# Optimization experiments

Measured on AMD Instinct MI355X. Metric: run time of the kernel, lower is better.

Reference implementation:

```python
import jax, jax.numpy as jnp
import numpy as np


def _mw_weight(m):
    if m == 1:
        return 1j * np.pi / 2
    if m == -1:
        return -1j * np.pi / 2
    if m % 2 == 0:
        return 2.0 / (1 - m * m)
    return 0.0


def quad_weights_mw(L):
    # Exact MW quadrature weights (McEwen & Wiaux 2011), folded to L theta samples.
    ms = np.arange(-(L - 1), L)
    w = np.array([_mw_weight(m) for m in ms], dtype=np.complex128)
    w *= np.exp(-1j * ms * np.pi / (2 * L - 1))
    wr = np.real(np.fft.fft(np.fft.ifftshift(w))) / (2 * L - 1)
    q = wr[:L].copy()
    q[: L - 1] += wr[2 * L - 2 : L - 1 : -1]  # fold extended-grid weights (spin=0)
    return q * 2 * np.pi / (2 * L - 1)


def legendre_table(L, theta):
    # Normalized assoc. Legendre Pbar_{lm}(cos theta) incl. sqrt((2l+1)/4pi (l-m)!/(l+m)!)
    # and Condon-Shortley phase. Returns (L, 2L-1, ntheta) with m index = m + L - 1.
    ct, st = np.cos(theta), np.sin(theta)
    nt = theta.shape[0]
    P = np.zeros((L, L, nt))
    P[0, 0] = 1.0 / np.sqrt(4 * np.pi)
    for m in range(1, L):
        P[m, m] = -np.sqrt((2 * m + 1) / (2.0 * m)) * st * P[m - 1, m - 1]
    for m in range(0, L - 1):
        P[m + 1, m] = np.sqrt(2 * m + 3.0) * ct * P[m, m]
    for m in range(0, L):
        for l in range(m + 2, L):
            a = np.sqrt((4.0 * l * l - 1) / (l * l - m * m))
            b = np.sqrt(((2.0 * l + 1) * ((l - 1) ** 2 - m * m)) / ((2.0 * l - 3) * (l * l - m * m)))
            P[l, m] = a * ct * P[l - 1, m] - b * P[l - 2, m]
    full = np.zeros((L, 2 * L - 1, nt))
    for m in range(0, L):
        full[:, L - 1 + m] = P[:, m]
        if m > 0:
            full[:, L - 1 - m] = ((-1) ** m) * P[:, m]
    return full


def _mw_theta(L):
    return np.pi * (2 * np.arange(L) + 1) / (2 * L - 1)


def sht_forward(f, L, plm, weights):
    # f: (L, 2L-1, C) real -> flm: (L, 2L-1, C) complex
    nphi = 2 * L - 1
    ms = np.arange(-(L - 1), L)
    Fm = jnp.fft.fft(f, axis=1)[:, ms % nphi, :]  # (ntheta, 2L-1, C)
    return jnp.einsum('t,lmt,tmc->lmc', weights, plm, Fm)


def sht_inverse(flm, L, plm):
    # flm: (L, 2L-1, C) complex -> real field (L, 2L-1, C)
    nphi = 2 * L - 1
    ms = np.arange(-(L - 1), L)
    G = jnp.einsum('lmc,lmt->tmc', flm, plm)  # (ntheta, 2L-1, C)
    Gfull = jnp.zeros_like(G).at[:, ms % nphi, :].set(G)
    return jnp.real(jnp.fft.ifft(Gfull, axis=1) * nphi)


def resize_flm(flm, L_new):
    L_old = flm.shape[0]
    if L_new == L_old:
        return flm
    if L_new < L_old:
        return flm[:L_new, L_old - L_new : L_old + L_new - 1]
    out = jnp.zeros((L_new, 2 * L_new - 1) + flm.shape[2:], flm.dtype)
    return out.at[:L_old, L_new - L_old : L_new + L_old - 1].set(flm)


def setup_inputs() -> dict:
    key = jax.random.key(0)
    ks = jax.random.split(key, 6)
    L_in, Lf, L_out = 128, 64, 128
    Cin, Cout, T = 64, 64, 256
    return {
        'x': jax.random.normal(ks[0], (L_in, 2 * L_in - 1, Cin), jnp.float32),
        't_emb': jax.random.normal(ks[1], (T,), jnp.float32),
        'A_real': 0.01 * jax.random.normal(ks[2], (Lf, 2 * Lf - 1, T), jnp.float32),
        'A_imag': 0.01 * jax.random.normal(ks[3], (Lf, 2 * Lf - 1, T), jnp.float32),
        'R_real': 0.01 * jax.random.normal(ks[4], (Lf, 2 * Lf - 1, Cout, Cin), jnp.float32),
        'R_imag': 0.01 * jax.random.normal(ks[5], (Lf, 2 * Lf - 1, Cout, Cin), jnp.float32),
        'L_out_spatial': L_out,
    }


def reference(x, t_emb, A_real, A_imag, R_real, R_imag, L_out_spatial):
    L_in = x.shape[0]
    Lf = A_real.shape[0]
    plm_in = jnp.asarray(legendre_table(L_in, _mw_theta(L_in)), jnp.float32)
    w_in = jnp.asarray(quad_weights_mw(L_in), jnp.float32)
    flm = sht_forward(x, L_in, plm_in, w_in)            # (L_in, 2L_in-1, Cin)
    flm = resize_flm(flm, Lf)                           # (Lf, 2Lf-1, Cin)
    t_c = (jnp.einsum('t,lmt->lm', t_emb, A_real)
           + 1j * jnp.einsum('t,lmt->lm', t_emb, A_imag))
    R = R_real + 1j * R_imag                            # (Lf, 2Lf-1, O, I)
    Rt = jnp.einsum('lm,lmoi->loi', t_c, R)
    flm_out = jnp.einsum('lmi,loi->lmo', flm, Rt)
    flm_out = resize_flm(flm_out, L_out_spatial)
    plm_out = jnp.asarray(legendre_table(L_out_spatial, _mw_theta(L_out_spatial)), jnp.float32)
    return sht_inverse(flm_out, L_out_spatial, plm_out)  # (L_out, 2L_out-1, O)
```

## Files before the change

### kernel.cpp

```cpp
#include <hip/hip_runtime.h>
#include <math.h>

#define PI_D 3.14159265358979323846
static const size_t OFF_P   = 0;
static const size_t OFF_W   = 524288;
static const size_t OFF_TW  = 524416;
static const size_t OFF_FMW = 524928;
static const size_t OFF_TC  = 1573504;
static const size_t OFF_FLM = 1589760;
static const size_t OFF_RT  = 2114048;
static const size_t OFF_FO  = 2638336;
static const size_t OFF_G   = 524928;
static const size_t WS_FLOATS = 3678720;

__global__ __launch_bounds__(256) void k_tables(float* __restrict__ w, float2* __restrict__ tw) {
  int t = blockIdx.x;
  int tid = threadIdx.x;
  if (t == 0 && tid < 255) {
    double a = 2.0 * PI_D * tid / 255.0;
    tw[tid] = make_float2((float)cos(a), (float)sin(a));
  }
  double term = 0.0;
  if (tid < 255) {
    int m = tid - 127;
    double br = 0.0, bi = 0.0; bool active = true;
    if (m == 1) bi = PI_D / 2.0;
    else if (m == -1) bi = -PI_D / 2.0;
    else if ((m & 1) == 0) br = 2.0 / (1.0 - (double)m * (double)m);
    else active = false;
    if (active) {
      double md = (double)m;
      double ca = cos(PI_D * md / 255.0), sa = -sin(PI_D * md / 255.0);
      double wr = br * ca - bi * sa;
      double wi = br * sa + bi * ca;
      double a1 = 2.0 * PI_D * md * t / 255.0;
      double fr = cos(a1), fi = -sin(a1);
      if (t < 127) {
        double a2 = 2.0 * PI_D * md * (t + 1) / 255.0;
        fr += cos(a2); fi += sin(a2);
      }
      term = wr * fr - wi * fi;
    }
  }
  __shared__ double red[256];
  red[tid] = term;
  __syncthreads();
  for (int off = 128; off; off >>= 1) {
    if (tid < off) red[tid] += red[tid + off];
    __syncthreads();
  }
  if (tid == 0) w[t] = (float)(red[0] * 2.0 * PI_D / (255.0 * 255.0));
}

__global__ __launch_bounds__(128) void k_legendre(float* __restrict__ P) {
  int m = blockIdx.x, t = threadIdx.x;
  double th = PI_D * (2 * t + 1) / 255.0;
  double ct = cos(th), st = sin(th);
  double pmm = 0.28209479177387814;
  for (int k = 1; k <= m; ++k) pmm *= -sqrt((2.0 * k + 1.0) / (2.0 * k)) * st;
  float* Pm = P + ((size_t)m * 64) * 128;
  Pm[(size_t)m * 128 + t] = (float)pmm;
  if (m + 1 < 64) {
    double p0 = pmm, p1 = sqrt(2.0 * m + 3.0) * ct * pmm;
    Pm[(size_t)(m + 1) * 128 + t] = (float)p1;
    for (int l = m + 2; l < 64; ++l) {
      double ll = (double)l * l, mm = (double)m * m;
      double a = sqrt((4.0 * ll - 1.0) / (ll - mm));
      double b = sqrt((2.0 * l + 1.0) * ((double)(l - 1) * (l - 1) - mm) / ((2.0 * l - 3.0) * (ll - mm)));
      double pl = a * ct * p1 - b * p0;
      Pm[(size_t)l * 128 + t] = (float)pl;
      p0 = p1; p1 = pl;
    }
  }
}

__global__ __launch_bounds__(256) void k_tc(const float* __restrict__ te, const float* __restrict__ Ar,
                                            const float* __restrict__ Ai, float2* __restrict__ tc) {
  int bid = blockIdx.x;
  int tid = threadIdx.x;
  float e = te[tid];
  float vr = Ar[(size_t)bid * 256 + tid] * e;
  float vi = Ai[(size_t)bid * 256 + tid] * e;
  for (int off = 32; off; off >>= 1) {
    vr += __shfl_down(vr, off);
    vi += __shfl_down(vi, off);
  }
  __shared__ float2 red[4];
  if ((tid & 63) == 0) red[tid >> 6] = make_float2(vr, vi);
  __syncthreads();
  if (tid == 0) {
    float2 s = red[0];
    for (int q = 1; q < 4; ++q) { s.x += red[q].x; s.y += red[q].y; }
    tc[bid] = s;
  }
}

__global__ __launch_bounds__(256) void k_fused(const float* __restrict__ x, const float* __restrict__ w,
                                               const float2* __restrict__ tw, float2* __restrict__ Fmw,
                                               const float* __restrict__ Rr, const float* __restrict__ Ri,
                                               const float2* __restrict__ tc, float2* __restrict__ Rt) {
  __shared__ union SM {
    float xs[64 * 64];
    struct {
      float2 tcs[127];
      float4 redr[256];
      float4 redi[256];
    } rt;
  } sm;
  int bid = blockIdx.x;
  int tid = threadIdx.x;
  int id = bid >> 1;

  if ((bid & 1) == 0) {
    int t = id >> 3, mq = id & 7;
    int c = tid & 63, ms = tid >> 6;
    int m0 = mq * 8 + ms * 2;
    float2 wm0 = tw[m0], wm1 = tw[m0 + 1];
    float cr0 = wm0.x, ci0 = -wm0.y;
    float cr1 = wm1.x, ci1 = -wm1.y;
    float tr0 = 1.f, ti0 = 0.f, tr1 = 1.f, ti1 = 0.f;
    float a0r = 0.f, a0i = 0.f, a1r = 0.f, a1i = 0.f;
    const float* xrow = x + (size_t)t * (255 * 64);
    for (int ch = 0; ch < 4; ++ch) {
      int plen = (ch == 3) ? 63 : 64;
      __syncthreads();
      const float4* src = reinterpret_cast<const float4*>(xrow + ch * 64 * 64);
      int n4 = plen * 16;
      for (int idx = tid; idx < n4; idx += 256)
        reinterpret_cast<float4*>(sm.xs)[idx] = src[idx];
      __syncthreads();
#pragma unroll 4
      for (int p = 0; p < plen; ++p) {
        float xv = sm.xs[p * 64 + c];
        a0r += xv * tr0; a0i += xv * ti0;
        a1r += xv * tr1; a1i += xv * ti1;
        float n0 = tr0 * cr0 - ti0 * ci0; ti0 = tr0 * ci0 + ti0 * cr0; tr0 = n0;
        float n1 = tr1 * cr1 - ti1 * ci1; ti1 = tr1 * ci1 + ti1 * cr1; tr1 = n1;
      }
    }
    float wt = w[t];
    Fmw[((size_t)m0 * 128 + t) * 64 + c] = make_float2(wt * a0r, wt * a0i);
    Fmw[((size_t)(m0 + 1) * 128 + t) * 64 + c] = make_float2(wt * a1r, wt * a1i);
  } else {
    int l = id >> 4, og = id & 15;
    if (tid < 127) sm.rt.tcs[tid] = tc[l * 127 + tid];
    __syncthreads();
    int slot = tid & 63;
    int jq = tid >> 6;
    int ic = slot & 15, ol = slot >> 4;
    int o = og * 4 + ol;
    const float* rr = Rr + ((size_t)l * 127) * 4096 + o * 64 + ic * 4;
    const float* ri = Ri + ((size_t)l * 127) * 4096 + o * 64 + ic * 4;
    float4 ar = make_float4(0.f, 0.f, 0.f, 0.f);
    float4 ai = make_float4(0.f, 0.f, 0.f, 0.f);
#pragma unroll 4
    for (int j = jq; j < 127; j += 4) {
      float2 w2 = sm.rt.tcs[j];
      float4 a = *reinterpret_cast<const float4*>(rr + (size_t)j * 4096);
      float4 b = *reinterpret_cast<const float4*>(ri + (size_t)j * 4096);
      ar.x += w2.x * a.x - w2.y * b.x;  ai.x += w2.x * b.x + w2.y * a.x;
      ar.y += w2.x * a.y - w2.y * b.y;  ai.y += w2.x * b.y + w2.y * a.y;
      ar.z += w2.x * a.z - w2.y * b.z;  ai.z += w2.x * b.z + w2.y * a.z;
      ar.w += w2.x * a.w - w2.y * b.w;  ai.w += w2.x * b.w + w2.y * a.w;
    }
    sm.rt.redr[tid] = ar; sm.rt.redi[tid] = ai;
    __syncthreads();
    if (jq == 0) {
#pragma unroll
      for (int q = 1; q < 4; ++q) {
        float4 a = sm.rt.redr[q * 64 + slot];
        float4 b = sm.rt.redi[q * 64 + slot];
        ar.x += a.x; ar.y += a.y; ar.z += a.z; ar.w += a.w;
        ai.x += b.x; ai.y += b.y; ai.z += b.z; ai.w += b.w;
      }
      float4* rt4 = reinterpret_cast<float4*>(Rt);
      size_t base = ((size_t)l * 64 + o) * 32 + ic * 2;
      rt4[base]     = make_float4(ar.x, ai.x, ar.y, ai.y);
      rt4[base + 1] = make_float4(ar.z, ai.z, ar.w, ai.w);
    }
  }
}

__global__ __launch_bounds__(256) void k_flm(const float* __restrict__ P, const float2* __restrict__ Fmw,
                                             float2* __restrict__ flm) {
  int m = blockIdx.x, lq = blockIdx.y;
  int tid = threadIdx.x;
  int c = tid & 63, lg = tid >> 6;
  __shared__ float2 Fs[32][64];
  __shared__ float Ps[8][32];
  float2 acc[2];
  acc[0] = make_float2(0.f, 0.f);
  acc[1] = make_float2(0.f, 0.f);
  for (int q = 0; q < 4; ++q) {
    __syncthreads();
    for (int idx = tid; idx < 2048; idx += 256) {
      int tt = idx >> 6, cc = idx & 63;
      Fs[tt][cc] = Fmw[((size_t)m * 128 + q * 32 + tt) * 64 + cc];
    }
    {
      int ll = tid >> 5, tt2 = tid & 31;
      int l = m + lq * 8 + ll;
      Ps[ll][tt2] = (l < 64) ? P[((size_t)m * 64 + l) * 128 + q * 32 + tt2] : 0.f;
    }
    __syncthreads();
    int li = lg * 2;
#pragma unroll 8
    for (int tt = 0; tt < 32; ++tt) {
      float2 f = Fs[tt][c];
      float p0 = Ps[li][tt], p1 = Ps[li + 1][tt];
      acc[0].x += p0 * f.x; acc[0].y += p0 * f.y;
      acc[1].x += p1 * f.x; acc[1].y += p1 * f.y;
    }
  }
#pragma unroll
  for (int s = 0; s < 2; ++s) {
    int l = m + lq * 8 + lg * 2 + s;
    if (l < 64) flm[((size_t)l * 64 + m) * 64 + c] = acc[s];
  }
}

__global__ __launch_bounds__(256) void k_flmout(const float2* __restrict__ flm, const float2* __restrict__ Rt,
                                                float2* __restrict__ fo) {
  int l = blockIdx.x, jg = blockIdx.y;
  int o = threadIdx.x & 63, js = threadIdx.x >> 6;
  __shared__ float2 Rts[64][65];
  __shared__ float2 Fjs[16][64];
  for (int idx = threadIdx.x; idx < 4096; idx += 256) {
    int oo = idx >> 6, ii = idx & 63;
    Rts[oo][ii] = Rt[((size_t)l * 64 + oo) * 64 + ii];
  }
  for (int idx = threadIdx.x; idx < 1024; idx += 256) {
    int jl = idx >> 6, ii = idx & 63;
    int j = jg * 16 + jl;
    float2 v = make_float2(0.f, 0.f);
    if (j < 127) {
      int mm = j - 63, am = mm < 0 ? -mm : mm;
      if (l >= am) {
        float2 f = flm[((size_t)l * 64 + am) * 64 + ii];
        if (mm < 0) { float s = (am & 1) ? -1.f : 1.f; v = make_float2(s * f.x, -s * f.y); }
        else v = f;
      }
    }
    Fjs[jl][ii] = v;
  }
  __syncthreads();
  float2 acc[4];
#pragma unroll
  for (int q = 0; q < 4; ++q) acc[q] = make_float2(0.f, 0.f);
  for (int i = 0; i < 64; ++i) {
    float2 r = Rts[o][i];
#pragma unroll
    for (int q = 0; q < 4; ++q) {
      float2 f = Fjs[js * 4 + q][i];
      acc[q].x += f.x * r.x - f.y * r.y;
      acc[q].y += f.x * r.y + f.y * r.x;
    }
  }
#pragma unroll
  for (int q = 0; q < 4; ++q) {
    int j = jg * 16 + js * 4 + q;
    if (j < 127) fo[((size_t)l * 127 + j) * 64 + o] = acc[q];
  }
}

__global__ __launch_bounds__(256) void k_g(const float* __restrict__ P, const float2* __restrict__ fo,
                                           float2* __restrict__ G) {
  int j = blockIdx.x, tg = blockIdx.y;
  int mm = j - 63, am = mm < 0 ? -mm : mm;
  float sgn = (mm < 0 && (am & 1)) ? -1.f : 1.f;
  int o = threadIdx.x & 63, ts = threadIdx.x >> 6;
  __shared__ float Ps[64][64];
  __shared__ float2 Fos[64][64];
  for (int idx = threadIdx.x; idx < 4096; idx += 256) {
    int ll = idx >> 6, tt = idx & 63;
    Ps[ll][tt] = P[((size_t)am * 64 + ll) * 128 + tg * 64 + tt];
  }
  for (int idx = threadIdx.x; idx < 4096; idx += 256) {
    int ll = idx >> 6, oo = idx & 63;
    float2 v = fo[((size_t)ll * 127 + j) * 64 + oo];
    Fos[ll][oo] = make_float2(sgn * v.x, sgn * v.y);
  }
  __syncthreads();
  float ar[16], ai2[16];
#pragma unroll
  for (int r = 0; r < 16; ++r) { ar[r] = 0.f; ai2[r] = 0.f; }
  for (int l = am; l < 64; ++l) {
    float2 f = Fos[l][o];
#pragma unroll
    for (int q = 0; q < 4; ++q) {
      float4 pv = *reinterpret_cast<const float4*>(&Ps[l][ts * 16 + q * 4]);
      ar[q * 4 + 0] += pv.x * f.x;  ai2[q * 4 + 0] += pv.x * f.y;
      ar[q * 4 + 1] += pv.y * f.x;  ai2[q * 4 + 1] += pv.y * f.y;
      ar[q * 4 + 2] += pv.z * f.x;  ai2[q * 4 + 2] += pv.z * f.y;
      ar[q * 4 + 3] += pv.w * f.x;  ai2[q * 4 + 3] += pv.w * f.y;
    }
  }
#pragma unroll
  for (int r = 0; r < 16; ++r) {
    int t = tg * 64 + ts * 16 + r;
    G[((size_t)t * 127 + j) * 64 + o] = make_float2(ar[r], ai2[r]);
  }
}

__global__ __launch_bounds__(256) void k_idft(const float2* __restrict__ G, const float2* __restrict__ tw,
                                              float* __restrict__ out) {
  int t = blockIdx.x, pq = blockIdx.y;
  int pl = threadIdx.x & 63, og = threadIdx.x >> 6;
  __shared__ __align__(16) unsigned char smem[65536];
  float2 (*CSs)[64] = reinterpret_cast<float2(*)[64]>(smem);
  float (*Ls)[65] = reinterpret_cast<float(*)[65]>(smem);
  for (int idx = threadIdx.x; idx < 4096; idx += 256) {
    int m = idx >> 6, oo = idx & 63;
    float2 v;
    if (m == 0) {
      float2 g = G[((size_t)t * 127 + 63) * 64 + oo];
      v = make_float2(g.x, 0.f);
    } else {
      float2 gp = G[((size_t)t * 127 + 63 + m) * 64 + oo];
      float2 gm = G[((size_t)t * 127 + 63 - m) * 64 + oo];
      v = make_float2(gp.x + gm.x, gm.y - gp.y);
    }
    CSs[m][oo] = v;
  }
  __syncthreads();
  int p = pq * 64 + pl;
  float2 wp = tw[p < 255 ? p : 0];
  float twr = 1.f, twi = 0.f;
  float acc[16];
#pragma unroll
  for (int r = 0; r < 16; ++r) acc[r] = 0.f;
  int ob = og * 16;
  for (int m = 0; m < 64; ++m) {
#pragma unroll
    for (int q = 0; q < 8; ++q) {
      float4 cs = *reinterpret_cast<const float4*>(&CSs[m][ob + q * 2]);
      acc[q * 2 + 0] += cs.x * twr + cs.y * twi;
      acc[q * 2 + 1] += cs.z * twr + cs.w * twi;
    }
    float nr = twr * wp.x - twi * wp.y;
    twi = twr * wp.y + twi * wp.x;
    twr = nr;
  }
  __syncthreads();
#pragma unroll
  for (int r = 0; r < 16; ++r) Ls[pl][ob + r] = acc[r];
  __syncthreads();
  for (int idx = threadIdx.x; idx < 4096; idx += 256) {
    int rr = idx >> 6, oo = idx & 63;
    int pg = pq * 64 + rr;
    if (pg < 255) out[((size_t)t * 255 + pg) * 64 + oo] = Ls[rr][oo];
  }
}

extern "C" void kernel_launch(void* const* d_in, const int* in_sizes, int n_in,
                              void* d_out, int out_size, void* d_ws, size_t ws_size,
                              hipStream_t stream) {
  (void)in_sizes; (void)n_in; (void)out_size;
  if (ws_size < WS_FLOATS * sizeof(float)) return;

  const float* x  = (const float*)d_in[0];
  const float* te = (const float*)d_in[1];
  const float* Ar = (const float*)d_in[2];
  const float* Ai = (const float*)d_in[3];
  const float* Rr = (const float*)d_in[4];
  const float* Ri = (const float*)d_in[5];
  float* out = (float*)d_out;

  float* ws = (float*)d_ws;
  float*  P   = ws + OFF_P;
  float*  w   = ws + OFF_W;
  float2* tw  = (float2*)(ws + OFF_TW);
  float2* Fmw = (float2*)(ws + OFF_FMW);
  float2* tc  = (float2*)(ws + OFF_TC);
  float2* flm = (float2*)(ws + OFF_FLM);
  float2* Rt  = (float2*)(ws + OFF_RT);
  float2* fo  = (float2*)(ws + OFF_FO);
  float2* G   = (float2*)(ws + OFF_G);

  k_tables<<<128, 256, 0, stream>>>(w, tw);
  k_legendre<<<64, 128, 0, stream>>>(P);
  k_tc<<<64 * 127, 256, 0, stream>>>(te, Ar, Ai, tc);
  k_fused<<<2048, 256, 0, stream>>>(x, w, tw, Fmw, Rr, Ri, tc, Rt);
  k_flm<<<dim3(64, 8), 256, 0, stream>>>(P, Fmw, flm);
  k_flmout<<<dim3(64, 8), 256, 0, stream>>>(flm, Rt, fo);
  k_g<<<dim3(127, 2), 256, 0, stream>>>(P, fo, G);
  k_idft<<<dim3(128, 4), 256, 0, stream>>>(G, tw, out);
}
```

Before: 390.8 us.

## Merge prep kernels and fuse tail stages into persistent kernel with grid barriers

Combines the table, Legendre and time-conditioning kernels into one launch, and replaces the four tail kernels (flm, flm_out, G, iDFT) with a single 512-block kernel that separates its stages with atomic grid-wide barriers. The G stage is re-split into 508 blocks with half the theta range each, so it occupies more of the grid. The goal is to remove launch gaps and per-kernel ramp-up and drain. The cost is spin-wait barriers, which rely on all 512 blocks being co-resident and could deadlock if they are not, plus a shared-memory union that may lower occupancy.

Measured after the change: 543.4 us. +39.1%, slower.

```diff
diff --git a/kernel.cpp b/kernel.cpp
--- a/kernel.cpp
+++ b/kernel.cpp
@@ -5,6 +5,7 @@
 static const size_t OFF_P   = 0;
 static const size_t OFF_W   = 524288;
 static const size_t OFF_TW  = 524416;
+static const size_t OFF_BAR = 524926;
 static const size_t OFF_FMW = 524928;
 static const size_t OFF_TC  = 1573504;
 static const size_t OFF_FLM = 1589760;
@@ -13,85 +14,95 @@
 static const size_t OFF_G   = 524928;
 static const size_t WS_FLOATS = 3678720;
 
-__global__ __launch_bounds__(256) void k_tables(float* __restrict__ w, float2* __restrict__ tw) {
-  int t = blockIdx.x;
-  int tid = threadIdx.x;
-  if (t == 0 && tid < 255) {
-    double a = 2.0 * PI_D * tid / 255.0;
-    tw[tid] = make_float2((float)cos(a), (float)sin(a));
-  }
-  double term = 0.0;
-  if (tid < 255) {
-    int m = tid - 127;
-    double br = 0.0, bi = 0.0; bool active = true;
-    if (m == 1) bi = PI_D / 2.0;
-    else if (m == -1) bi = -PI_D / 2.0;
-    else if ((m & 1) == 0) br = 2.0 / (1.0 - (double)m * (double)m);
-    else active = false;
-    if (active) {
-      double md = (double)m;
-      double ca = cos(PI_D * md / 255.0), sa = -sin(PI_D * md / 255.0);
-      double wr = br * ca - bi * sa;
-      double wi = br * sa + bi * ca;
-      double a1 = 2.0 * PI_D * md * t / 255.0;
-      double fr = cos(a1), fi = -sin(a1);
-      if (t < 127) {
-        double a2 = 2.0 * PI_D * md * (t + 1) / 255.0;
-        fr += cos(a2); fi += sin(a2);
-      }
-      term = wr * fr - wi * fi;
-    }
-  }
-  __shared__ double red[256];
-  red[tid] = term;
-  __syncthreads();
-  for (int off = 128; off; off >>= 1) {
-    if (tid < off) red[tid] += red[tid + off];
-    __syncthreads();
-  }
-  if (tid == 0) w[t] = (float)(red[0] * 2.0 * PI_D / (255.0 * 255.0));
-}
-
-__global__ __launch_bounds__(128) void k_legendre(float* __restrict__ P) {
-  int m = blockIdx.x, t = threadIdx.x;
-  double th = PI_D * (2 * t + 1) / 255.0;
-  double ct = cos(th), st = sin(th);
-  double pmm = 0.28209479177387814;
-  for (int k = 1; k <= m; ++k) pmm *= -sqrt((2.0 * k + 1.0) / (2.0 * k)) * st;
-  float* Pm = P + ((size_t)m * 64) * 128;
-  Pm[(size_t)m * 128 + t] = (float)pmm;
-  if (m + 1 < 64) {
-    double p0 = pmm, p1 = sqrt(2.0 * m + 3.0) * ct * pmm;
-    Pm[(size_t)(m + 1) * 128 + t] = (float)p1;
-    for (int l = m + 2; l < 64; ++l) {
-      double ll = (double)l * l, mm = (double)m * m;
-      double a = sqrt((4.0 * ll - 1.0) / (ll - mm));
-      double b = sqrt((2.0 * l + 1.0) * ((double)(l - 1) * (l - 1) - mm) / ((2.0 * l - 3.0) * (ll - mm)));
-      double pl = a * ct * p1 - b * p0;
-      Pm[(size_t)l * 128 + t] = (float)pl;
-      p0 = p1; p1 = pl;
-    }
-  }
-}
-
-__global__ __launch_bounds__(256) void k_tc(const float* __restrict__ te, const float* __restrict__ Ar,
-                                            const float* __restrict__ Ai, float2* __restrict__ tc) {
-  int bid = blockIdx.x;
-  int tid = threadIdx.x;
-  float e = te[tid];
-  float vr = Ar[(size_t)bid * 256 + tid] * e;
-  float vi = Ai[(size_t)bid * 256 + tid] * e;
-  for (int off = 32; off; off >>= 1) {
-    vr += __shfl_down(vr, off);
-    vi += __shfl_down(vi, off);
-  }
-  __shared__ float2 red[4];
-  if ((tid & 63) == 0) red[tid >> 6] = make_float2(vr, vi);
-  __syncthreads();
-  if (tid == 0) {
-    float2 s = red[0];
-    for (int q = 1; q < 4; ++q) { s.x += red[q].x; s.y += red[q].y; }
-    tc[bid] = s;
+#define NBLK_TAIL 512
+
+__global__ __launch_bounds__(256) void k_prep(float* __restrict__ w, float2* __restrict__ tw,
+                                              float* __restrict__ P,
+                                              const float* __restrict__ te, const float* __restrict__ Ar,
+                                              const float* __restrict__ Ai, float2* __restrict__ tc,
+                                              unsigned* __restrict__ bar) {
+  __shared__ double redd[256];
+  __shared__ float2 red2[4];
+  int bid = blockIdx.x, tid = threadIdx.x;
+
+  if (bid < 128) {
+    int t = bid;
+    if (t == 0 && tid == 0) bar[0] = 0u;
+    if (t == 0 && tid < 255) {
+      double a = 2.0 * PI_D * tid / 255.0;
+      tw[tid] = make_float2((float)cos(a), (float)sin(a));
+    }
+    double term = 0.0;
+    if (tid < 255) {
+      int m = tid - 127;
+      double br = 0.0, bi = 0.0; bool active = true;
+      if (m == 1) bi = PI_D / 2.0;
+      else if (m == -1) bi = -PI_D / 2.0;
+      else if ((m & 1) == 0) br = 2.0 / (1.0 - (double)m * (double)m);
+      else active = false;
+      if (active) {
+        double md = (double)m;
+        double ca = cos(PI_D * md / 255.0), sa = -sin(PI_D * md / 255.0);
+        double wr = br * ca - bi * sa;
+        double wi = br * sa + bi * ca;
+        double a1 = 2.0 * PI_D * md * t / 255.0;
+        double fr = cos(a1), fi = -sin(a1);
+        if (t < 127) {
+          double a2 = 2.0 * PI_D * md * (t + 1) / 255.0;
+          fr += cos(a2); fi += sin(a2);
+        }
+        term = wr * fr - wi * fi;
+      }
+    }
+    redd[tid] = term;
+    __syncthreads();
+    for (int off = 128; off; off >>= 1) {
+      if (tid < off) redd[tid] += redd[tid + off];
+      __syncthreads();
+    }
+    if (tid == 0) w[t] = (float)(redd[0] * 2.0 * PI_D / (255.0 * 255.0));
+  } else if (bid < 192) {
+    if (tid < 128) {
+      int m = bid - 128, t = tid;
+      double th = PI_D * (2 * t + 1) / 255.0;
+      double ct = cos(th), st = sin(th);
+      double pmm = 0.28209479177387814;
+      for (int k = 1; k <= m; ++k) pmm *= -sqrt((2.0 * k + 1.0) / (2.0 * k)) * st;
+      float* Pm = P + ((size_t)m * 64) * 128;
+      Pm[(size_t)m * 128 + t] = (float)pmm;
+      if (m + 1 < 64) {
+        double p0 = pmm, p1 = sqrt(2.0 * m + 3.0) * ct * pmm;
+        Pm[(size_t)(m + 1) * 128 + t] = (float)p1;
+        for (int l = m + 2; l < 64; ++l) {
+          double ll = (double)l * l, mm = (double)m * m;
+          double a = sqrt((4.0 * ll - 1.0) / (ll - mm));
+          double b = sqrt((2.0 * l + 1.0) * ((double)(l - 1) * (l - 1) - mm) / ((2.0 * l - 3.0) * (ll - mm)));
+          double pl = a * ct * p1 - b * p0;
+          Pm[(size_t)l * 128 + t] = (float)pl;
+          p0 = p1; p1 = pl;
+        }
+      }
+    }
+  } else {
+    int b = bid - 192;
+    float e = te[tid];
+    for (int k = 0; k < 16; ++k) {
+      int pair = b * 16 + k;
+      float vr = Ar[(size_t)pair * 256 + tid] * e;
+      float vi = Ai[(size_t)pair * 256 + tid] * e;
+      for (int off = 32; off; off >>= 1) {
+        vr += __shfl_down(vr, off);
+        vi += __shfl_down(vi, off);
+      }
+      if ((tid & 63) == 0) red2[tid >> 6] = make_float2(vr, vi);
+      __syncthreads();
+      if (tid == 0) {
+        float2 s = red2[0];
+        for (int q = 1; q < 4; ++q) { s.x += red2[q].x; s.y += red2[q].y; }
+        tc[pair] = s;
+      }
+      __syncthreads();
+    }
   }
 }
 
@@ -181,174 +192,188 @@
   }
 }
 
-__global__ __launch_bounds__(256) void k_flm(const float* __restrict__ P, const float2* __restrict__ Fmw,
-                                             float2* __restrict__ flm) {
-  int m = blockIdx.x, lq = blockIdx.y;
-  int tid = threadIdx.x;
-  int c = tid & 63, lg = tid >> 6;
-  __shared__ float2 Fs[32][64];
-  __shared__ float Ps[8][32];
-  float2 acc[2];
-  acc[0] = make_float2(0.f, 0.f);
-  acc[1] = make_float2(0.f, 0.f);
-  for (int q = 0; q < 4; ++q) {
-    __syncthreads();
+__device__ __forceinline__ void grid_bar(unsigned* bar, unsigned target) {
+  __syncthreads();
+  if (threadIdx.x == 0) {
+    __threadfence();
+    __hip_atomic_fetch_add(bar, 1u, __ATOMIC_ACQ_REL, __HIP_MEMORY_SCOPE_AGENT);
+    while (__hip_atomic_load(bar, __ATOMIC_ACQUIRE, __HIP_MEMORY_SCOPE_AGENT) < target)
+      __builtin_amdgcn_s_sleep(2);
+    __threadfence();
+  }
+  __syncthreads();
+}
+
+__global__ __launch_bounds__(256, 2) void k_tail(const float* __restrict__ P, const float2* __restrict__ Fmw,
+                                                 float2* __restrict__ flm, const float2* __restrict__ Rt,
+                                                 float2* __restrict__ fo, float2* __restrict__ G,
+                                                 const float2* __restrict__ tw, float* __restrict__ out,
+                                                 unsigned* __restrict__ bar) {
+  __shared__ union TSM {
+    struct { float2 Fs[32][64]; float Ps[8][32]; } flm;
+    struct { float2 Rts[64][65]; float2 Fjs[16][64]; } fo;
+    struct { float Ps[64][32]; float2 Fos[64][64]; } g;
+    struct { float2 CSs[64][64]; float Ls[64][65]; } idft;
+  } sm;
+  int bid = blockIdx.x, tid = threadIdx.x;
+
+  {
+    int m = bid >> 3, lq = bid & 7;
+    int c = tid & 63, lg = tid >> 6;
+    float2 acc[2];
+    acc[0] = make_float2(0.f, 0.f);
+    acc[1] = make_float2(0.f, 0.f);
+    for (int q = 0; q < 4; ++q) {
+      __syncthreads();
+      for (int idx = tid; idx < 2048; idx += 256) {
+        int tt = idx >> 6, cc = idx & 63;
+        sm.flm.Fs[tt][cc] = Fmw[((size_t)m * 128 + q * 32 + tt) * 64 + cc];
+      }
+      {
+        int ll = tid >> 5, tt2 = tid & 31;
+        int l = m + lq * 8 + ll;
+        sm.flm.Ps[ll][tt2] = (l < 64) ? P[((size_t)m * 64 + l) * 128 + q * 32 + tt2] : 0.f;
+      }
+      __syncthreads();
+      int li = lg * 2;
+#pragma unroll 8
+      for (int tt = 0; tt < 32; ++tt) {
+        float2 f = sm.flm.Fs[tt][c];
+        float p0 = sm.flm.Ps[li][tt], p1 = sm.flm.Ps[li + 1][tt];
+        acc[0].x += p0 * f.x; acc[0].y += p0 * f.y;
+        acc[1].x += p1 * f.x; acc[1].y += p1 * f.y;
+      }
+    }
+#pragma unroll
+    for (int s = 0; s < 2; ++s) {
+      int l = m + lq * 8 + lg * 2 + s;
+      if (l < 64) flm[((size_t)l * 64 + m) * 64 + c] = acc[s];
+    }
+  }
+  grid_bar(bar, NBLK_TAIL);
+
+  {
+    int l = bid >> 3, jg = bid & 7;
+    int o = tid & 63, js = tid >> 6;
+    for (int idx = tid; idx < 4096; idx += 256) {
+      int oo = idx >> 6, ii = idx & 63;
+      sm.fo.Rts[oo][ii] = Rt[((size_t)l * 64 + oo) * 64 + ii];
+    }
+    for (int idx = tid; idx < 1024; idx += 256) {
+      int jl = idx >> 6, ii = idx & 63;
+      int j = jg * 16 + jl;
+      float2 v = make_float2(0.f, 0.f);
+      if (j < 127) {
+        int mm = j - 63, am = mm < 0 ? -mm : mm;
+        if (l >= am) {
+          float2 f = flm[((size_t)l * 64 + am) * 64 + ii];
+          if (mm < 0) { float s = (am & 1) ? -1.f : 1.f; v = make_float2(s * f.x, -s * f.y); }
+          else v = f;
+        }
+      }
+      sm.fo.Fjs[jl][ii] = v;
+    }
+    __syncthreads();
+    float2 acc[4];
+#pragma unroll
+    for (int q = 0; q < 4; ++q) acc[q] = make_float2(0.f, 0.f);
+    for (int i = 0; i < 64; ++i) {
+      float2 r = sm.fo.Rts[o][i];
+#pragma unroll
+      for (int q = 0; q < 4; ++q) {
+        float2 f = sm.fo.Fjs[js * 4 + q][i];
+        acc[q].x += f.x * r.x - f.y * r.y;
+        acc[q].y += f.x * r.y + f.y * r.x;
+      }
+    }
+#pragma unroll
+    for (int q = 0; q < 4; ++q) {
+      int j = jg * 16 + js * 4 + q;
+      if (j < 127) fo[((size_t)l * 127 + j) * 64 + o] = acc[q];
+    }
+  }
+  grid_bar(bar, 2 * NBLK_TAIL);
+
+  if (bid < 508) {
+    int j = bid >> 2, tg = bid & 3;
+    int mm = j - 63, am = mm < 0 ? -mm : mm;
+    float sgn = (mm < 0 && (am & 1)) ? -1.f : 1.f;
+    int o = tid & 63, ts = tid >> 6;
     for (int idx = tid; idx < 2048; idx += 256) {
-      int tt = idx >> 6, cc = idx & 63;
-      Fs[tt][cc] = Fmw[((size_t)m * 128 + q * 32 + tt) * 64 + cc];
-    }
-    {
-      int ll = tid >> 5, tt2 = tid & 31;
-      int l = m + lq * 8 + ll;
-      Ps[ll][tt2] = (l < 64) ? P[((size_t)m * 64 + l) * 128 + q * 32 + tt2] : 0.f;
-    }
-    __syncthreads();
-    int li = lg * 2;
-#pragma unroll 8
-    for (int tt = 0; tt < 32; ++tt) {
-      float2 f = Fs[tt][c];
-      float p0 = Ps[li][tt], p1 = Ps[li + 1][tt];
-      acc[0].x += p0 * f.x; acc[0].y += p0 * f.y;
-      acc[1].x += p1 * f.x; acc[1].y += p1 * f.y;
-    }
-  }
-#pragma unroll
-  for (int s = 0; s < 2; ++s) {
-    int l = m + lq * 8 + lg * 2 + s;
-    if (l < 64) flm[((size_t)l * 64 + m) * 64 + c] = acc[s];
-  }
-}
-
-__global__ __launch_bounds__(256) void k_flmout(const float2* __restrict__ flm, const float2* __restrict__ Rt,
-                                                float2* __restrict__ fo) {
-  int l = blockIdx.x, jg = blockIdx.y;
-  int o = threadIdx.x & 63, js = threadIdx.x >> 6;
-  __shared__ float2 Rts[64][65];
-  __shared__ float2 Fjs[16][64];
-  for (int idx = threadIdx.x; idx < 4096; idx += 256) {
-    int oo = idx >> 6, ii = idx & 63;
-    Rts[oo][ii] = Rt[((size_t)l * 64 + oo) * 64 + ii];
-  }
-  for (int idx = threadIdx.x; idx < 1024; idx += 256) {
-    int jl = idx >> 6, ii = idx & 63;
-    int j = jg * 16 + jl;
-    float2 v = make_float2(0.f, 0.f);
-    if (j < 127) {
-      int mm = j - 63, am = mm < 0 ? -mm : mm;
-      if (l >= am) {
-        float2 f = flm[((size_t)l * 64 + am) * 64 + ii];
-        if (mm < 0) { float s = (am & 1) ? -1.f : 1.f; v = make_float2(s * f.x, -s * f.y); }
-        else v = f;
-      }
-    }
-    Fjs[jl][ii] = v;
-  }
-  __syncthreads();
-  float2 acc[4];
-#pragma unroll
-  for (int q = 0; q < 4; ++q) acc[q] = make_float2(0.f, 0.f);
-  for (int i = 0; i < 64; ++i) {
-    float2 r = Rts[o][i];
-#pragma unroll
-    for (int q = 0; q < 4; ++q) {
-      float2 f = Fjs[js * 4 + q][i];
-      acc[q].x += f.x * r.x - f.y * r.y;
-      acc[q].y += f.x * r.y + f.y * r.x;
-    }
-  }
-#pragma unroll
-  for (int q = 0; q < 4; ++q) {
-    int j = jg * 16 + js * 4 + q;
-    if (j < 127) fo[((size_t)l * 127 + j) * 64 + o] = acc[q];
-  }
-}
-
-__global__ __launch_bounds__(256) void k_g(const float* __restrict__ P, const float2* __restrict__ fo,
-                                           float2* __restrict__ G) {
-  int j = blockIdx.x, tg = blockIdx.y;
-  int mm = j - 63, am = mm < 0 ? -mm : mm;
-  float sgn = (mm < 0 && (am & 1)) ? -1.f : 1.f;
-  int o = threadIdx.x & 63, ts = threadIdx.x >> 6;
-  __shared__ float Ps[64][64];
-  __shared__ float2 Fos[64][64];
-  for (int idx = threadIdx.x; idx < 4096; idx += 256) {
-    int ll = idx >> 6, tt = idx & 63;
-    Ps[ll][tt] = P[((size_t)am * 64 + ll) * 128 + tg * 64 + tt];
-  }
-  for (int idx = threadIdx.x; idx < 4096; idx += 256) {
-    int ll = idx >> 6, oo = idx & 63;
-    float2 v = fo[((size_t)ll * 127 + j) * 64 + oo];
-    Fos[ll][oo] = make_float2(sgn * v.x, sgn * v.y);
-  }
-  __syncthreads();
-  float ar[16], ai2[16];
-#pragma unroll
-  for (int r = 0; r < 16; ++r) { ar[r] = 0.f; ai2[r] = 0.f; }
-  for (int l = am; l < 64; ++l) {
-    float2 f = Fos[l][o];
-#pragma unroll
-    for (int q = 0; q < 4; ++q) {
-      float4 pv = *reinterpret_cast<const float4*>(&Ps[l][ts * 16 + q * 4]);
-      ar[q * 4 + 0] += pv.x * f.x;  ai2[q * 4 + 0] += pv.x * f.y;
-      ar[q * 4 + 1] += pv.y * f.x;  ai2[q * 4 + 1] += pv.y * f.y;
-      ar[q * 4 + 2] += pv.z * f.x;  ai2[q * 4 + 2] += pv.z * f.y;
-      ar[q * 4 + 3] += pv.w * f.x;  ai2[q * 4 + 3] += pv.w * f.y;
-    }
-  }
-#pragma unroll
-  for (int r = 0; r < 16; ++r) {
-    int t = tg * 64 + ts * 16 + r;
-    G[((size_t)t * 127 + j) * 64 + o] = make_float2(ar[r], ai2[r]);
-  }
-}
-
-__global__ __launch_bounds__(256) void k_idft(const float2* __restrict__ G, const float2* __restrict__ tw,
-                                              float* __restrict__ out) {
-  int t = blockIdx.x, pq = blockIdx.y;
-  int pl = threadIdx.x & 63, og = threadIdx.x >> 6;
-  __shared__ __align__(16) unsigned char smem[65536];
-  float2 (*CSs)[64] = reinterpret_cast<float2(*)[64]>(smem);
-  float (*Ls)[65] = reinterpret_cast<float(*)[65]>(smem);
-  for (int idx = threadIdx.x; idx < 4096; idx += 256) {
-    int m = idx >> 6, oo = idx & 63;
-    float2 v;
-    if (m == 0) {
-      float2 g = G[((size_t)t * 127 + 63) * 64 + oo];
-      v = make_float2(g.x, 0.f);
-    } else {
-      float2 gp = G[((size_t)t * 127 + 63 + m) * 64 + oo];
-      float2 gm = G[((size_t)t * 127 + 63 - m) * 64 + oo];
-      v = make_float2(gp.x + gm.x, gm.y - gp.y);
-    }
-    CSs[m][oo] = v;
-  }
-  __syncthreads();
-  int p = pq * 64 + pl;
-  float2 wp = tw[p < 255 ? p : 0];
-  float twr = 1.f, twi = 0.f;
-  float acc[16];
-#pragma unroll
-  for (int r = 0; r < 16; ++r) acc[r] = 0.f;
-  int ob = og * 16;
-  for (int m = 0; m < 64; ++m) {
-#pragma unroll
-    for (int q = 0; q < 8; ++q) {
-      float4 cs = *reinterpret_cast<const float4*>(&CSs[m][ob + q * 2]);
-      acc[q * 2 + 0] += cs.x * twr + cs.y * twi;
-      acc[q * 2 + 1] += cs.z * twr + cs.w * twi;
-    }
-    float nr = twr * wp.x - twi * wp.y;
-    twi = twr * wp.y + twi * wp.x;
-    twr = nr;
-  }
-  __syncthreads();
-#pragma unroll
-  for (int r = 0; r < 16; ++r) Ls[pl][ob + r] = acc[r];
-  __syncthreads();
-  for (int idx = threadIdx.x; idx < 4096; idx += 256) {
-    int rr = idx >> 6, oo = idx & 63;
-    int pg = pq * 64 + rr;
-    if (pg < 255) out[((size_t)t * 255 + pg) * 64 + oo] = Ls[rr][oo];
+      int ll = idx >> 5, tt = idx & 31;
+      sm.g.Ps[ll][tt] = P[((size_t)am * 64 + ll) * 128 + tg * 32 + tt];
+    }
+    for (int idx = tid; idx < 4096; idx += 256) {
+      int ll = idx >> 6, oo = idx & 63;
+      float2 v = fo[((size_t)ll * 127 + j) * 64 + oo];
+      sm.g.Fos[ll][oo] = make_float2(sgn * v.x, sgn * v.y);
+    }
+    __syncthreads();
+    float ar[8], ai2[8];
+#pragma unroll
+    for (int r = 0; r < 8; ++r) { ar[r] = 0.f; ai2[r] = 0.f; }
+    for (int l = am; l < 64; ++l) {
+      float2 f = sm.g.Fos[l][o];
+#pragma unroll
+      for (int q = 0; q < 2; ++q) {
+        float4 pv = *reinterpret_cast<const float4*>(&sm.g.Ps[l][ts * 8 + q * 4]);
+        ar[q * 4 + 0] += pv.x * f.x;  ai2[q * 4 + 0] += pv.x * f.y;
+        ar[q * 4 + 1] += pv.y * f.x;  ai2[q * 4 + 1] += pv.y * f.y;
+        ar[q * 4 + 2] += pv.z * f.x;  ai2[q * 4 + 2] += pv.z * f.y;
+        ar[q * 4 + 3] += pv.w * f.x;  ai2[q * 4 + 3] += pv.w * f.y;
+      }
+    }
+#pragma unroll
+    for (int r = 0; r < 8; ++r) {
+      int t = tg * 32 + ts * 8 + r;
+      G[((size_t)t * 127 + j) * 64 + o] = make_float2(ar[r], ai2[r]);
+    }
+  }
+  grid_bar(bar, 3 * NBLK_TAIL);
+
+  {
+    int t = bid >> 2, pq = bid & 3;
+    int pl = tid & 63, og = tid >> 6;
+    for (int idx = tid; idx < 4096; idx += 256) {
+      int m = idx >> 6, oo = idx & 63;
+      float2 v;
+      if (m == 0) {
+        float2 g = G[((size_t)t * 127 + 63) * 64 + oo];
+        v = make_float2(g.x, 0.f);
+      } else {
+        float2 gp = G[((size_t)t * 127 + 63 + m) * 64 + oo];
+        float2 gm = G[((size_t)t * 127 + 63 - m) * 64 + oo];
+        v = make_float2(gp.x + gm.x, gm.y - gp.y);
+      }
+      sm.idft.CSs[m][oo] = v;
+    }
+    __syncthreads();
+    int p = pq * 64 + pl;
+    float2 wp = tw[p < 255 ? p : 0];
+    float twr = 1.f, twi = 0.f;
+    float acc[16];
+#pragma unroll
+    for (int r = 0; r < 16; ++r) acc[r] = 0.f;
+    int ob = og * 16;
+    for (int m = 0; m < 64; ++m) {
+#pragma unroll
+      for (int q = 0; q < 8; ++q) {
+        float4 cs = *reinterpret_cast<const float4*>(&sm.idft.CSs[m][ob + q * 2]);
+        acc[q * 2 + 0] += cs.x * twr + cs.y * twi;
+        acc[q * 2 + 1] += cs.z * twr + cs.w * twi;
+      }
+      float nr = twr * wp.x - twi * wp.y;
+      twi = twr * wp.y + twi * wp.x;
+      twr = nr;
+    }
+#pragma unroll
+    for (int r = 0; r < 16; ++r) sm.idft.Ls[pl][ob + r] = acc[r];
+    __syncthreads();
+    for (int idx = tid; idx < 4096; idx += 256) {
+      int rr = idx >> 6, oo = idx & 63;
+      int pg = pq * 64 + rr;
+      if (pg < 255) out[((size_t)t * 255 + pg) * 64 + oo] = sm.idft.Ls[rr][oo];
+    }
   }
 }
 
@@ -367,22 +392,18 @@
   float* out = (float*)d_out;
 
   float* ws = (float*)d_ws;
-  float*  P   = ws + OFF_P;
-  float*  w   = ws + OFF_W;
-  float2* tw  = (float2*)(ws + OFF_TW);
-  float2* Fmw = (float2*)(ws + OFF_FMW);
-  float2* tc  = (float2*)(ws + OFF_TC);
-  float2* flm = (float2*)(ws + OFF_FLM);
-  float2* Rt  = (float2*)(ws + OFF_RT);
-  float2* fo  = (float2*)(ws + OFF_FO);
-  float2* G   = (float2*)(ws + OFF_G);
-
-  k_tables<<<128, 256, 0, stream>>>(w, tw);
-  k_legendre<<<64, 128, 0, stream>>>(P);
-  k_tc<<<64 * 127, 256, 0, stream>>>(te, Ar, Ai, tc);
+  float*    P   = ws + OFF_P;
+  float*    w   = ws + OFF_W;
+  float2*   tw  = (float2*)(ws + OFF_TW);
+  unsigned* bar = (unsigned*)(ws + OFF_BAR);
+  float2*   Fmw = (float2*)(ws + OFF_FMW);
+  float2*   tc  = (float2*)(ws + OFF_TC);
+  float2*   flm = (float2*)(ws + OFF_FLM);
+  float2*   Rt  = (float2*)(ws + OFF_RT);
+  float2*   fo  = (float2*)(ws + OFF_FO);
+  float2*   G   = (float2*)(ws + OFF_G);
+
+  k_prep<<<700, 256, 0, stream>>>(w, tw, P, te, Ar, Ai, tc, bar);
   k_fused<<<2048, 256, 0, stream>>>(x, w, tw, Fmw, Rr, Ri, tc, Rt);
-  k_flm<<<dim3(64, 8), 256, 0, stream>>>(P, Fmw, flm);
-  k_flmout<<<dim3(64, 8), 256, 0, stream>>>(flm, Rt, fo);
-  k_g<<<dim3(127, 2), 256, 0, stream>>>(P, fo, G);
-  k_idft<<<dim3(128, 4), 256, 0, stream>>>(G, tw, out);
+  k_tail<<<NBLK_TAIL, 256, 0, stream>>>(P, Fmw, flm, Rt, fo, G, tw, out, bar);
 }
```

## Merge table, Legendre and t_c kernels into one launch; nontemporal R loads

Applied to the files above, without the earlier changes.

Folds the three setup kernels (quadrature weights and twiddles, Legendre table, t_c reduction) into a single 700-block kernel that dispatches on block index. Each t_c block now handles 16 (l,m) pairs instead of one. This removes two kernel launches and lets the independent setup work run concurrently. Separately, the large R_real/R_imag streaming loads in the fused kernel switch to nontemporal loads to reduce cache pollution. The trade-off is imbalance inside the merged kernel, since the double-precision Legendre blocks are long-running while the other blocks are short.

After: 370.5 us. 5.2% less time.

```diff
diff --git a/kernel.cpp b/kernel.cpp
--- a/kernel.cpp
+++ b/kernel.cpp
@@ -13,85 +13,93 @@
 static const size_t OFF_G   = 524928;
 static const size_t WS_FLOATS = 3678720;
 
-__global__ __launch_bounds__(256) void k_tables(float* __restrict__ w, float2* __restrict__ tw) {
-  int t = blockIdx.x;
-  int tid = threadIdx.x;
-  if (t == 0 && tid < 255) {
-    double a = 2.0 * PI_D * tid / 255.0;
-    tw[tid] = make_float2((float)cos(a), (float)sin(a));
-  }
-  double term = 0.0;
-  if (tid < 255) {
-    int m = tid - 127;
-    double br = 0.0, bi = 0.0; bool active = true;
-    if (m == 1) bi = PI_D / 2.0;
-    else if (m == -1) bi = -PI_D / 2.0;
-    else if ((m & 1) == 0) br = 2.0 / (1.0 - (double)m * (double)m);
-    else active = false;
-    if (active) {
-      double md = (double)m;
-      double ca = cos(PI_D * md / 255.0), sa = -sin(PI_D * md / 255.0);
-      double wr = br * ca - bi * sa;
-      double wi = br * sa + bi * ca;
-      double a1 = 2.0 * PI_D * md * t / 255.0;
-      double fr = cos(a1), fi = -sin(a1);
-      if (t < 127) {
-        double a2 = 2.0 * PI_D * md * (t + 1) / 255.0;
-        fr += cos(a2); fi += sin(a2);
-      }
-      term = wr * fr - wi * fi;
-    }
-  }
-  __shared__ double red[256];
-  red[tid] = term;
-  __syncthreads();
-  for (int off = 128; off; off >>= 1) {
-    if (tid < off) red[tid] += red[tid + off];
-    __syncthreads();
-  }
-  if (tid == 0) w[t] = (float)(red[0] * 2.0 * PI_D / (255.0 * 255.0));
-}
-
-__global__ __launch_bounds__(128) void k_legendre(float* __restrict__ P) {
-  int m = blockIdx.x, t = threadIdx.x;
-  double th = PI_D * (2 * t + 1) / 255.0;
-  double ct = cos(th), st = sin(th);
-  double pmm = 0.28209479177387814;
-  for (int k = 1; k <= m; ++k) pmm *= -sqrt((2.0 * k + 1.0) / (2.0 * k)) * st;
-  float* Pm = P + ((size_t)m * 64) * 128;
-  Pm[(size_t)m * 128 + t] = (float)pmm;
-  if (m + 1 < 64) {
-    double p0 = pmm, p1 = sqrt(2.0 * m + 3.0) * ct * pmm;
-    Pm[(size_t)(m + 1) * 128 + t] = (float)p1;
-    for (int l = m + 2; l < 64; ++l) {
-      double ll = (double)l * l, mm = (double)m * m;
-      double a = sqrt((4.0 * ll - 1.0) / (ll - mm));
-      double b = sqrt((2.0 * l + 1.0) * ((double)(l - 1) * (l - 1) - mm) / ((2.0 * l - 3.0) * (ll - mm)));
-      double pl = a * ct * p1 - b * p0;
-      Pm[(size_t)l * 128 + t] = (float)pl;
-      p0 = p1; p1 = pl;
-    }
-  }
-}
-
-__global__ __launch_bounds__(256) void k_tc(const float* __restrict__ te, const float* __restrict__ Ar,
-                                            const float* __restrict__ Ai, float2* __restrict__ tc) {
-  int bid = blockIdx.x;
-  int tid = threadIdx.x;
-  float e = te[tid];
-  float vr = Ar[(size_t)bid * 256 + tid] * e;
-  float vi = Ai[(size_t)bid * 256 + tid] * e;
-  for (int off = 32; off; off >>= 1) {
-    vr += __shfl_down(vr, off);
-    vi += __shfl_down(vi, off);
-  }
-  __shared__ float2 red[4];
-  if ((tid & 63) == 0) red[tid >> 6] = make_float2(vr, vi);
-  __syncthreads();
-  if (tid == 0) {
-    float2 s = red[0];
-    for (int q = 1; q < 4; ++q) { s.x += red[q].x; s.y += red[q].y; }
-    tc[bid] = s;
+typedef float vf4 __attribute__((ext_vector_type(4)));
+
+__global__ __launch_bounds__(256) void k_prep(float* __restrict__ w, float2* __restrict__ tw,
+                                              float* __restrict__ P,
+                                              const float* __restrict__ te, const float* __restrict__ Ar,
+                                              const float* __restrict__ Ai, float2* __restrict__ tc) {
+  __shared__ double redd[256];
+  __shared__ float2 red2[4];
+  int bid = blockIdx.x, tid = threadIdx.x;
+
+  if (bid < 128) {
+    int t = bid;
+    if (t == 0 && tid < 255) {
+      double a = 2.0 * PI_D * tid / 255.0;
+      tw[tid] = make_float2((float)cos(a), (float)sin(a));
+    }
+    double term = 0.0;
+    if (tid < 255) {
+      int m = tid - 127;
+      double br = 0.0, bi = 0.0; bool active = true;
+      if (m == 1) bi = PI_D / 2.0;
+      else if (m == -1) bi = -PI_D / 2.0;
+      else if ((m & 1) == 0) br = 2.0 / (1.0 - (double)m * (double)m);
+      else active = false;
+      if (active) {
+        double md = (double)m;
+        double ca = cos(PI_D * md / 255.0), sa = -sin(PI_D * md / 255.0);
+        double wr = br * ca - bi * sa;
+        double wi = br * sa + bi * ca;
+        double a1 = 2.0 * PI_D * md * t / 255.0;
+        double fr = cos(a1), fi = -sin(a1);
+        if (t < 127) {
+          double a2 = 2.0 * PI_D * md * (t + 1) / 255.0;
+          fr += cos(a2); fi += sin(a2);
+        }
+        term = wr * fr - wi * fi;
+      }
+    }
+    redd[tid] = term;
+    __syncthreads();
+    for (int off = 128; off; off >>= 1) {
+      if (tid < off) redd[tid] += redd[tid + off];
+      __syncthreads();
+    }
+    if (tid == 0) w[t] = (float)(redd[0] * 2.0 * PI_D / (255.0 * 255.0));
+  } else if (bid < 192) {
+    if (tid < 128) {
+      int m = bid - 128, t = tid;
+      double th = PI_D * (2 * t + 1) / 255.0;
+      double ct = cos(th), st = sin(th);
+      double pmm = 0.28209479177387814;
+      for (int k = 1; k <= m; ++k) pmm *= -sqrt((2.0 * k + 1.0) / (2.0 * k)) * st;
+      float* Pm = P + ((size_t)m * 64) * 128;
+      Pm[(size_t)m * 128 + t] = (float)pmm;
+      if (m + 1 < 64) {
+        double p0 = pmm, p1 = sqrt(2.0 * m + 3.0) * ct * pmm;
+        Pm[(size_t)(m + 1) * 128 + t] = (float)p1;
+        for (int l = m + 2; l < 64; ++l) {
+          double ll = (double)l * l, mm = (double)m * m;
+          double a = sqrt((4.0 * ll - 1.0) / (ll - mm));
+          double b = sqrt((2.0 * l + 1.0) * ((double)(l - 1) * (l - 1) - mm) / ((2.0 * l - 3.0) * (ll - mm)));
+          double pl = a * ct * p1 - b * p0;
+          Pm[(size_t)l * 128 + t] = (float)pl;
+          p0 = p1; p1 = pl;
+        }
+      }
+    }
+  } else {
+    int b = bid - 192;
+    float e = te[tid];
+    for (int k = 0; k < 16; ++k) {
+      int pair = b * 16 + k;
+      float vr = Ar[(size_t)pair * 256 + tid] * e;
+      float vi = Ai[(size_t)pair * 256 + tid] * e;
+      for (int off = 32; off; off >>= 1) {
+        vr += __shfl_down(vr, off);
+        vi += __shfl_down(vi, off);
+      }
+      if ((tid & 63) == 0) red2[tid >> 6] = make_float2(vr, vi);
+      __syncthreads();
+      if (tid == 0) {
+        float2 s = red2[0];
+        for (int q = 1; q < 4; ++q) { s.x += red2[q].x; s.y += red2[q].y; }
+        tc[pair] = s;
+      }
+      __syncthreads();
+    }
   }
 }
 
@@ -156,8 +164,8 @@
 #pragma unroll 4
     for (int j = jq; j < 127; j += 4) {
       float2 w2 = sm.rt.tcs[j];
-      float4 a = *reinterpret_cast<const float4*>(rr + (size_t)j * 4096);
-      float4 b = *reinterpret_cast<const float4*>(ri + (size_t)j * 4096);
+      vf4 a = __builtin_nontemporal_load(reinterpret_cast<const vf4*>(rr + (size_t)j * 4096));
+      vf4 b = __builtin_nontemporal_load(reinterpret_cast<const vf4*>(ri + (size_t)j * 4096));
       ar.x += w2.x * a.x - w2.y * b.x;  ai.x += w2.x * b.x + w2.y * a.x;
       ar.y += w2.x * a.y - w2.y * b.y;  ai.y += w2.x * b.y + w2.y * a.y;
       ar.z += w2.x * a.z - w2.y * b.z;  ai.z += w2.x * b.z + w2.y * a.z;
@@ -377,9 +385,7 @@
   float2* fo  = (float2*)(ws + OFF_FO);
   float2* G   = (float2*)(ws + OFF_G);
 
-  k_tables<<<128, 256, 0, stream>>>(w, tw);
-  k_legendre<<<64, 128, 0, stream>>>(P);
-  k_tc<<<64 * 127, 256, 0, stream>>>(te, Ar, Ai, tc);
+  k_prep<<<700, 256, 0, stream>>>(w, tw, P, te, Ar, Ai, tc);
   k_fused<<<2048, 256, 0, stream>>>(x, w, tw, Fmw, Rr, Ri, tc, Rt);
   k_flm<<<dim3(64, 8), 256, 0, stream>>>(P, Fmw, flm);
   k_flmout<<<dim3(64, 8), 256, 0, stream>>>(flm, Rt, fo);
```
